# Kernel optimization log

Measured on AMD Instinct MI355X. Metric: run time of the kernel, lower is better.

## Reference

```python
import jax, jax.numpy as jnp
import numpy as np

N = 262144   # total packed tokens
B = 4096     # number of ragged segments
D = 256      # relation_embed_dim
A = 128      # attention_dim


def setup_inputs() -> dict:
    key = jax.random.key(0)
    k1, k2, k3 = jax.random.split(key, 3)
    relation_embeds = jax.random.normal(k1, (N, D), dtype=jnp.float32)
    # ragged segment ends: B-1 random interior end positions + final position N-1
    rng = np.random.default_rng(0)
    ends = np.sort(rng.choice(N - 1, size=B - 1, replace=False))
    ends = np.concatenate([ends, [N - 1]])
    queries_np = np.zeros((N,), dtype=np.int32)
    queries_np[ends] = 1
    queries = jnp.asarray(queries_np)
    # torch nn.Linear weights: [out, in]
    Wq = jax.random.normal(k2, (A, D), dtype=jnp.float32) / np.sqrt(D)
    Wk = jax.random.normal(k3, (A, D), dtype=jnp.float32) / np.sqrt(D)
    return {"relation_embeds": relation_embeds, "queries": queries,
            "num_segments": B, "Wq": Wq, "Wk": Wk}


def reference(relation_embeds, queries, num_segments, Wq, Wk):
    # segment id per token: exclusive cumsum of end markers
    q = queries.astype(jnp.int32)
    seg = jnp.cumsum(q) - q                      # [N] in [0, num_segments)
    ends = jnp.flatnonzero(q, size=num_segments) # [B] last index of each segment
    # per-segment query = Q(last row of segment); per-token key = K(row)
    q_end = relation_embeds[ends] @ Wq.T         # [B, A]
    k = relation_embeds @ Wk.T                   # [N, A]
    logits = jnp.sum(k * q_end[seg], axis=-1)    # [N] dot(Q_seg, K_token)
    # softmax over each ragged segment (dim=0 within segment)
    m = jax.ops.segment_max(logits, seg, num_segments=num_segments)
    ex = jnp.exp(logits - m[seg])
    denom = jax.ops.segment_sum(ex, seg, num_segments=num_segments)
    return ex / denom[seg]                       # [N] concatenated scores
```

## Files before the change

kernel.cpp:

```cpp
#include <hip/hip_runtime.h>
#include <math.h>
#include <float.h>

constexpr int N = 262144;
constexpr int B = 4096;
constexpr int D = 256;
constexpr int A = 128;

constexpr int CHUNK  = 1024;
constexpr int NCHUNK = N / CHUNK;
constexpr int SEGB   = 8;

__global__ void k_partials_M(const int* __restrict__ q, int* __restrict__ partials,
                             const float* __restrict__ Wq, const float* __restrict__ Wk,
                             float* __restrict__ M) {
    int t = threadIdx.x;
    if (blockIdx.x < NCHUNK) {
        int4 v = ((const int4*)q)[blockIdx.x * (CHUNK / 4) + t];
        int s = v.x + v.y + v.z + v.w;
        __shared__ int sm[256];
        sm[t] = s; __syncthreads();
        for (int o = 128; o > 0; o >>= 1) {
            if (t < o) sm[t] += sm[t + o];
            __syncthreads();
        }
        if (t == 0) partials[blockIdx.x] = sm[0];
    } else {
        int d1 = blockIdx.x - NCHUNK;
        int d2 = t;
        float acc = 0.f;
#pragma unroll 4
        for (int a = 0; a < A; a++) {
            acc = fmaf(Wk[a * D + d1], Wq[a * D + d2], acc);
        }
        M[d1 * D + d2] = acc;
    }
}

__global__ void k_seg_ends(const int* __restrict__ q, const int* __restrict__ partials,
                           int* __restrict__ seg, int* __restrict__ ends) {
    int t = threadIdx.x;
    int bid = blockIdx.x;
    __shared__ int sp[256];
    __shared__ int sm[256];
    sp[t] = partials[t];
    int4 v = ((const int4*)q)[bid * (CHUNK / 4) + t];
    int tsum = v.x + v.y + v.z + v.w;
    sm[t] = tsum;
    __syncthreads();
    for (int o = 1; o < 256; o <<= 1) {
        int a1 = (t >= o) ? sp[t - o] : 0;
        int a2 = (t >= o) ? sm[t - o] : 0;
        __syncthreads();
        sp[t] += a1;
        sm[t] += a2;
        __syncthreads();
    }
    int offs = (bid == 0) ? 0 : sp[bid - 1];
    int run = offs + sm[t] - tsum;
    int base_idx = bid * CHUNK + t * 4;
    int qq[4] = {v.x, v.y, v.z, v.w};
#pragma unroll
    for (int k = 0; k < 4; k++) {
        int idx = base_idx + k;
        seg[idx] = run;
        if (qq[k]) { ends[run] = idx; run++; }
    }
}

__global__ void k_compute_V(const float* __restrict__ X, const int* __restrict__ ends,
                            const float* __restrict__ M, float* __restrict__ V) {
    int t = threadIdx.x;
    int b0 = blockIdx.x * SEGB;
    const float4* xr[SEGB];
#pragma unroll
    for (int r = 0; r < SEGB; r++) {
        xr[r] = (const float4*)(X + (size_t)ends[b0 + r] * D);
    }
    const float4* Mrow = (const float4*)(M + t * D);
    float acc[SEGB];
#pragma unroll
    for (int r = 0; r < SEGB; r++) acc[r] = 0.f;
#pragma unroll 4
    for (int j = 0; j < D / 4; j++) {
        float4 m4 = Mrow[j];
#pragma unroll
        for (int r = 0; r < SEGB; r++) {
            float4 x4 = xr[r][j];
            acc[r] = fmaf(m4.x, x4.x, fmaf(m4.y, x4.y,
                     fmaf(m4.z, x4.z, fmaf(m4.w, x4.w, acc[r]))));
        }
    }
#pragma unroll
    for (int r = 0; r < SEGB; r++) V[(size_t)(b0 + r) * D + t] = acc[r];
}

__global__ void k_logits(const float* __restrict__ X, const int* __restrict__ seg,
                         const float* __restrict__ V, float* __restrict__ logits) {
    int wave = threadIdx.x >> 6;
    int lane = threadIdx.x & 63;
    int tok = blockIdx.x * 4 + wave;
    float4 x4 = ((const float4*)(X + (size_t)tok * D))[lane];
    int s = seg[tok];
    float4 v4 = ((const float4*)(V + (size_t)s * D))[lane];
    float p = fmaf(x4.x, v4.x, fmaf(x4.y, v4.y, fmaf(x4.z, v4.z, x4.w * v4.w)));
#pragma unroll
    for (int o = 32; o > 0; o >>= 1) p += __shfl_xor(p, o, 64);
    if (lane == 0) logits[tok] = p;
}

__global__ void k_softmax(const float* __restrict__ logits, const int* __restrict__ ends,
                          float* __restrict__ out) {
    int wave = threadIdx.x >> 6;
    int lane = threadIdx.x & 63;
    int b = blockIdx.x * 4 + wave;
    int start = (b == 0) ? 0 : (ends[b - 1] + 1);
    int end = ends[b];
    float m = -FLT_MAX, s = 0.f;
    for (int i = start + lane; i <= end; i += 64) {
        float x = logits[i];
        float nm = fmaxf(m, x);
        s = s * __expf(m - nm) + __expf(x - nm);
        m = nm;
    }
#pragma unroll
    for (int o = 32; o > 0; o >>= 1) {
        float mo = __shfl_xor(m, o, 64);
        float so = __shfl_xor(s, o, 64);
        float nm = fmaxf(m, mo);
        s = s * __expf(m - nm) + so * __expf(mo - nm);
        m = nm;
    }
    float r = 1.f / s;
    for (int i = start + lane; i <= end; i += 64) out[i] = __expf(logits[i] - m) * r;
}

extern "C" void kernel_launch(void* const* d_in, const int* in_sizes, int n_in,
                              void* d_out, int out_size, void* d_ws, size_t ws_size,
                              hipStream_t stream) {
    const float* X  = (const float*)d_in[0];
    const int*   q  = (const int*)d_in[1];
    const float* Wq = (const float*)d_in[3];
    const float* Wk = (const float*)d_in[4];
    float* out = (float*)d_out;

    char* ws = (char*)d_ws;
    size_t off = 0;
    auto alloc = [&](size_t bytes) -> char* {
        char* p = ws + off;
        off += (bytes + 255) & ~(size_t)255;
        return p;
    };
    int*   seg      = (int*)alloc((size_t)N * 4);
    int*   ends     = (int*)alloc((size_t)B * 4);
    int*   partials = (int*)alloc((size_t)NCHUNK * 4);
    float* M        = (float*)alloc((size_t)D * D * 4);
    float* V        = (float*)alloc((size_t)B * D * 4);
    float* logits   = (float*)alloc((size_t)N * 4);

    k_partials_M<<<NCHUNK + D, 256, 0, stream>>>(q, partials, Wq, Wk, M);
    k_seg_ends<<<NCHUNK, 256, 0, stream>>>(q, partials, seg, ends);
    k_compute_V<<<B / SEGB, 256, 0, stream>>>(X, ends, M, V);
    k_logits<<<N / 4, 256, 0, stream>>>(X, seg, V, logits);
    k_softmax<<<B / 4, 256, 0, stream>>>(logits, ends, out);
}
```

Baseline: 413.8 us.

## Use wave shuffles for scans and process two tokens per wave in logits

The shared-memory tree reduction and the Hillis-Steele scans are replaced with wavefront shuffle reductions and scans, which cuts the number of block-wide barriers. The logits kernel now handles two tokens per wave, uses nontemporal loads for X, and stores both results as one float2, halving the grid size. The intent is to reduce synchronisation overhead and increase memory-level parallelism in the main bandwidth-bound pass. In exchange, per-thread register use goes up, and nontemporal loads could change how caching behaves.

```diff
diff --git a/kernel.cpp b/kernel.cpp
--- a/kernel.cpp
+++ b/kernel.cpp
@@ -11,6 +11,8 @@
 constexpr int NCHUNK = N / CHUNK;
 constexpr int SEGB   = 8;
 
+typedef float fvec4 __attribute__((ext_vector_type(4)));
+
 __global__ void k_partials_M(const int* __restrict__ q, int* __restrict__ partials,
                              const float* __restrict__ Wq, const float* __restrict__ Wk,
                              float* __restrict__ M) {
@@ -18,13 +20,13 @@
     if (blockIdx.x < NCHUNK) {
         int4 v = ((const int4*)q)[blockIdx.x * (CHUNK / 4) + t];
         int s = v.x + v.y + v.z + v.w;
-        __shared__ int sm[256];
-        sm[t] = s; __syncthreads();
-        for (int o = 128; o > 0; o >>= 1) {
-            if (t < o) sm[t] += sm[t + o];
-            __syncthreads();
-        }
-        if (t == 0) partials[blockIdx.x] = sm[0];
+        int lane = t & 63, w = t >> 6;
+#pragma unroll
+        for (int o = 32; o > 0; o >>= 1) s += __shfl_xor(s, o, 64);
+        __shared__ int ws_[4];
+        if (lane == 0) ws_[w] = s;
+        __syncthreads();
+        if (t == 0) partials[blockIdx.x] = ws_[0] + ws_[1] + ws_[2] + ws_[3];
     } else {
         int d1 = blockIdx.x - NCHUNK;
         int d2 = t;
@@ -40,24 +42,33 @@
 __global__ void k_seg_ends(const int* __restrict__ q, const int* __restrict__ partials,
                            int* __restrict__ seg, int* __restrict__ ends) {
     int t = threadIdx.x;
+    int lane = t & 63, w = t >> 6;
     int bid = blockIdx.x;
-    __shared__ int sp[256];
-    __shared__ int sm[256];
-    sp[t] = partials[t];
+    int p = partials[t];
     int4 v = ((const int4*)q)[bid * (CHUNK / 4) + t];
     int tsum = v.x + v.y + v.z + v.w;
-    sm[t] = tsum;
+    int ps = p, ts = tsum;
+#pragma unroll
+    for (int o = 1; o < 64; o <<= 1) {
+        int po = __shfl_up(ps, o, 64);
+        int to = __shfl_up(ts, o, 64);
+        if (lane >= o) { ps += po; ts += to; }
+    }
+    __shared__ int wp[4], wt[4];
+    __shared__ int offs_sm;
+    if (lane == 63) { wp[w] = ps; wt[w] = ts; }
     __syncthreads();
-    for (int o = 1; o < 256; o <<= 1) {
-        int a1 = (t >= o) ? sp[t - o] : 0;
-        int a2 = (t >= o) ? sm[t - o] : 0;
-        __syncthreads();
-        sp[t] += a1;
-        sm[t] += a2;
-        __syncthreads();
+    int addp = 0, addt = 0;
+#pragma unroll
+    for (int i = 0; i < 4; i++) {
+        if (i < w) { addp += wp[i]; addt += wt[i]; }
     }
-    int offs = (bid == 0) ? 0 : sp[bid - 1];
-    int run = offs + sm[t] - tsum;
+    int sp_incl = ps + addp;
+    int sm_incl = ts + addt;
+    if (bid > 0 && t == bid - 1) offs_sm = sp_incl;
+    if (bid == 0 && t == 0) offs_sm = 0;
+    __syncthreads();
+    int run = offs_sm + sm_incl - tsum;
     int base_idx = bid * CHUNK + t * 4;
     int qq[4] = {v.x, v.y, v.z, v.w};
 #pragma unroll
@@ -99,14 +110,26 @@
                          const float* __restrict__ V, float* __restrict__ logits) {
     int wave = threadIdx.x >> 6;
     int lane = threadIdx.x & 63;
-    int tok = blockIdx.x * 4 + wave;
-    float4 x4 = ((const float4*)(X + (size_t)tok * D))[lane];
-    int s = seg[tok];
-    float4 v4 = ((const float4*)(V + (size_t)s * D))[lane];
-    float p = fmaf(x4.x, v4.x, fmaf(x4.y, v4.y, fmaf(x4.z, v4.z, x4.w * v4.w)));
+    int tok0 = (blockIdx.x * 4 + wave) * 2;
+    const fvec4* xa_p = (const fvec4*)(X + (size_t)tok0 * D) + lane;
+    const fvec4* xb_p = (const fvec4*)(X + (size_t)(tok0 + 1) * D) + lane;
+    fvec4 xa = __builtin_nontemporal_load(xa_p);
+    fvec4 xb = __builtin_nontemporal_load(xb_p);
+    int sa = seg[tok0];
+    int sb = seg[tok0 + 1];
+    float4 va = ((const float4*)(V + (size_t)sa * D))[lane];
+    float4 vb = ((const float4*)(V + (size_t)sb * D))[lane];
+    float pa = fmaf(xa.x, va.x, fmaf(xa.y, va.y, fmaf(xa.z, va.z, xa.w * va.w)));
+    float pb = fmaf(xb.x, vb.x, fmaf(xb.y, vb.y, fmaf(xb.z, vb.z, xb.w * vb.w)));
 #pragma unroll
-    for (int o = 32; o > 0; o >>= 1) p += __shfl_xor(p, o, 64);
-    if (lane == 0) logits[tok] = p;
+    for (int o = 32; o > 0; o >>= 1) {
+        pa += __shfl_xor(pa, o, 64);
+        pb += __shfl_xor(pb, o, 64);
+    }
+    if (lane == 0) {
+        float2 r = make_float2(pa, pb);
+        *((float2*)(logits + tok0)) = r;
+    }
 }
 
 __global__ void k_softmax(const float* __restrict__ logits, const int* __restrict__ ends,
@@ -161,6 +184,6 @@
     k_partials_M<<<NCHUNK + D, 256, 0, stream>>>(q, partials, Wq, Wk, M);
     k_seg_ends<<<NCHUNK, 256, 0, stream>>>(q, partials, seg, ends);
     k_compute_V<<<B / SEGB, 256, 0, stream>>>(X, ends, M, V);
-    k_logits<<<N / 4, 256, 0, stream>>>(X, seg, V, logits);
+    k_logits<<<N / 8, 256, 0, stream>>>(X, seg, V, logits);
     k_softmax<<<B / 4, 256, 0, stream>>>(logits, ends, out);
 }
```

New measurement: 406.5 us. Within noise of the previous version (-1.8%).
